# Performance work log

Hardware: AMD Instinct MI355X
Metric: run time of the kernel (lower is better)

Reference implementation:

```python
import jax, jax.numpy as jnp
import numpy as np

B, T, D, H = 64, 512, 1024, 1024


def setup_inputs() -> dict:
    key = jax.random.key(0)
    k1, k2, k3, k4, k5 = jax.random.split(key, 5)
    return {
        "c0": jax.random.normal(k1, (B, H), jnp.float32),
        "h0": jax.random.normal(k2, (B, H), jnp.float32),
        "x": jax.random.normal(k3, (B, T, D), jnp.float32),
        "Wi": jax.random.normal(k4, (D, 4 * H), jnp.float32) * 0.02,
        "Wh": jax.random.normal(k5, (H, 4 * H), jnp.float32) * 0.02,
        "b": jnp.zeros((4 * H,), jnp.float32),
    }


def reference(c0, h0, x, Wi, Wh, b):
    # flax OptimizedLSTMCell: fused gates = x @ Wi (no bias) + h @ Wh + b,
    # split into i, f, g, o; carry = (c, h).
    def step(carry, xt):
        c, h = carry
        gates = xt @ Wi + h @ Wh + b  # [B, 4H]
        i, f, g, o = jnp.split(gates, 4, axis=-1)
        new_c = jax.nn.sigmoid(f) * c + jax.nn.sigmoid(i) * jnp.tanh(g)
        new_h = jax.nn.sigmoid(o) * jnp.tanh(new_c)
        return (new_c, new_h), new_h

    # scan over time axis (original uses in_axes=1/out_axes=1)
    (cT, hT), ys = jax.lax.scan(step, (c0, h0), jnp.swapaxes(x, 0, 1))
    return cT, hT, jnp.swapaxes(ys, 0, 1)  # final carry + [B, T, H] outputs
```

## Files before the change

kernel.cpp:

```cpp
#include <hip/hip_runtime.h>

#define B_ 64
#define T_ 512
#define D_ 1024
#define H_ 1024
#define NG_ 4096

typedef __attribute__((ext_vector_type(8))) short short8v;
typedef __attribute__((ext_vector_type(4))) float f32x4;

static __device__ inline unsigned short f2bf(float f) {
  unsigned u = __float_as_uint(f);
  return (unsigned short)((u + 0x7fffu + ((u >> 16) & 1u)) >> 16);
}
static __device__ inline float bf2f(unsigned short s) {
  return __uint_as_float((unsigned)s << 16);
}

static __device__ inline float4 llc_load4(const float* p) {
  float4 r;
  asm volatile("global_load_dwordx4 %0, %1, off sc0 sc1" : "=v"(r) : "v"(p));
  return r;
}
static __device__ inline void llc_store1(float* p, float v) {
  asm volatile("global_store_dword %0, %1, off sc0 sc1" :: "v"(p), "v"(v) : "memory");
}
static __device__ inline void llc_store_u16(unsigned short* p, unsigned v) {
  asm volatile("global_store_short %0, %1, off sc0 sc1" :: "v"(p), "v"(v) : "memory");
}
#define VMWAIT(N)                                          \
  asm volatile("s_waitcnt vmcnt(" #N ")" ::: "memory");    \
  __builtin_amdgcn_sched_barrier(0);

__global__ __launch_bounds__(256) void k_trans_h_fwd(const float* __restrict__ h,
                                                     float* __restrict__ hT) {
  int idx = blockIdx.x * 256 + threadIdx.x;
  int b = idx & 63;
  int k = idx >> 6;
  hT[idx] = h[b * H_ + k];
}
__global__ __launch_bounds__(256) void k_trans_h_back(const float* __restrict__ hT,
                                                      float* __restrict__ h) {
  int idx = blockIdx.x * 256 + threadIdx.x;
  int k = idx & (H_ - 1);
  int b = idx >> 10;
  h[idx] = hT[k * 64 + b];
}

__global__ __launch_bounds__(256) void k_init_hfrag(const float* __restrict__ h0,
                                                    unsigned short* __restrict__ hf) {
  const int idx = blockIdx.x * 256 + threadIdx.x;
  const int j = idx & 7;
  const int l = (idx >> 3) & 63;
  const int bt = (idx >> 9) & 3;
  const int kt = idx >> 11;
  const int b = bt * 16 + (l & 15);
  const int k = kt * 32 + ((l >> 4) << 3) + j;
  hf[idx] = f2bf(h0[b * H_ + k]);
}

__global__ __launch_bounds__(256) void k_h_final(const float* __restrict__ ys,
                                                 float* __restrict__ h) {
  const int idx = blockIdx.x * 256 + threadIdx.x;
  const int b = idx >> 10;
  const int k = idx & 1023;
  h[idx] = ys[(size_t)b * (T_ * H_) + (size_t)(T_ - 1) * H_ + k];
}

__global__ __launch_bounds__(256) void k_prep_w(const float* __restrict__ Wi,
                                                short8v* __restrict__ wh) {
  const int idx = blockIdx.x * 256 + threadIdx.x;
  const int l = idx & 63;
  const int kt = (idx >> 6) & 31;
  const int nt = idx >> 11;
  const int n = nt * 16 + (l & 15);
  const int k = kt * 32 + ((l >> 4) << 3);
  short8v h;
#pragma unroll
  for (int j = 0; j < 8; ++j) h[j] = (short)f2bf(Wi[(size_t)(k + j) * NG_ + n]);
  wh[idx] = h;
}

__global__ __launch_bounds__(256) void k_prep_x(const float* __restrict__ x,
                                                short8v* __restrict__ xh,
                                                int t0) {
  const int idx = blockIdx.x * 256 + threadIdx.x;
  const int l = idx & 63;
  const int bt = (idx >> 6) & 3;
  const int kt = (idx >> 8) & 31;
  const int tt = idx >> 13;
  const int b = bt * 16 + (l & 15);
  const int k = kt * 32 + ((l >> 4) << 3);
  const float* p = x + ((size_t)b * T_ + (t0 + tt)) * D_ + k;
  const float4 f0 = *(const float4*)p;
  const float4 f1 = *(const float4*)(p + 4);
  const float v[8] = {f0.x, f0.y, f0.z, f0.w, f1.x, f1.y, f1.z, f1.w};
  short8v h;
#pragma unroll
  for (int j = 0; j < 8; ++j) h[j] = (short)f2bf(v[j]);
  xh[idx] = h;
}

__global__ __launch_bounds__(512, 2) void k_fused(
    const float* __restrict__ Wh,
    const short8v* __restrict__ xh,
    const short8v* __restrict__ wh,
    const float* __restrict__ bias,
    float* __restrict__ gx,
    unsigned short* __restrict__ hfA, unsigned short* __restrict__ hfB,
    float* __restrict__ c_state,
    float* __restrict__ ys,
    unsigned* __restrict__ bar,
    int t0, int tc) {
  extern __shared__ char smemc[];

  const int tid = threadIdx.x;
  const int l = tid & 63;
  const int w = tid >> 6;
  const int bid = blockIdx.x;
  unsigned* done = bar + 512;

  if (bid >= 128) {
    const int gi = bid - 128;
    const int oct = gi & 7;
    const int nt0 = oct * 32 + w * 4;
    for (int j = gi; j < tc * 8; j += 128) {
      const int tt = j >> 3;
      f32x4 acc[4][4];
#pragma unroll
      for (int i = 0; i < 4; ++i)
#pragma unroll
        for (int q = 0; q < 4; ++q) acc[i][q] = (f32x4){0.f, 0.f, 0.f, 0.f};

#pragma unroll 2
      for (int kt = 0; kt < 32; ++kt) {
        short8v ah[4], bh[4];
#pragma unroll
        for (int bt = 0; bt < 4; ++bt)
          ah[bt] = xh[((size_t)(tt * 32 + kt) * 4 + bt) * 64 + l];
#pragma unroll
        for (int q = 0; q < 4; ++q)
          bh[q] = wh[((size_t)(nt0 + q) * 32 + kt) * 64 + l];
#pragma unroll
        for (int bt = 0; bt < 4; ++bt)
#pragma unroll
          for (int q = 0; q < 4; ++q)
            acc[bt][q] = __builtin_amdgcn_mfma_f32_16x16x32_bf16(ah[bt], bh[q], acc[bt][q], 0, 0, 0);
      }

#pragma unroll
      for (int q = 0; q < 4; ++q) {
        const int n = (nt0 + q) * 16 + (l & 15);
        const int g = n >> 10;
        const int cb = (n & 1023) >> 2;
        const int c = n & 3;
        const float bv = bias[n];
#pragma unroll
        for (int bt = 0; bt < 4; ++bt)
#pragma unroll
          for (int r = 0; r < 4; ++r) {
            const int b = bt * 16 + (l >> 4) * 4 + r;
            llc_store1(gx + (((size_t)tt * 256 + cb) * 64 + b) * 16 + c * 4 + g,
                       acc[bt][q][r] + bv);
          }
      }
      asm volatile("s_waitcnt vmcnt(0)" ::: "memory");
      __syncthreads();
      if (tid == 0)
        __hip_atomic_fetch_add(&done[t0 + tt], 1u, __ATOMIC_RELAXED,
                               __HIP_MEMORY_SCOPE_AGENT);
    }
    return;
  }

  short8v* wldsh = (short8v*)smemc;
  short8v* wldsl = wldsh + 4096;
  float* red = (float*)(wldsl + 4096);

  const int bt = w & 3;
  const int kt0 = (w >> 2) * 16;
  const int hbase = bid * 8;

  for (int idx = tid; idx < 4096; idx += 512) {
    const int ct = idx >> 11;
    const int rem = idx & 2047;
    const int kt = rem >> 6;
    const int ll = rem & 63;
    const int cc = ll & 15;
    const int gc = ct * 16 + cc;
    const int c = gc >> 2, g = gc & 3;
    const int kb = kt * 32 + ((ll >> 4) << 3);
    short8v hi, lo;
#pragma unroll
    for (int j = 0; j < 8; ++j) {
      const float v = Wh[(size_t)(kb + j) * NG_ + g * H_ + hbase + c];
      const unsigned short bh = f2bf(v);
      hi[j] = (short)bh;
      lo[j] = (short)f2bf(v - bf2f(bh));
    }
    wldsh[idx] = hi;
    wldsl[idx] = lo;
  }

  const int eb = tid >> 3;
  const int c8 = tid & 7;
  const int hcol = hbase + c8;
  const size_t sOff = (((size_t)((hcol >> 5) * 4 + (eb >> 4)) * 64 +
                        ((((hcol & 31) >> 3) << 4) | (eb & 15))) * 8 + (hcol & 7));
  const int cbq = bid * 2 + (c8 >> 2);
  const int ebt = eb >> 4;
  const int erb = eb & 15;
  const int err_ = erb & 3;
  const int elrow = (erb >> 2) << 4;
  const int ect = c8 >> 2;

  float c_reg = c_state[eb * H_ + hcol];

  if (tid == 0) {
    while (__hip_atomic_load(&done[t0], __ATOMIC_RELAXED, __HIP_MEMORY_SCOPE_AGENT) < 8u)
      __builtin_amdgcn_s_sleep(1);
  }
  __syncthreads();

  for (int tt = 0; tt < tc; ++tt) {
    const int t = t0 + tt;
    const unsigned short* __restrict__ hf_in = (t & 1) ? hfB : hfA;
    unsigned short* __restrict__ hf_out = (t & 1) ? hfA : hfB;

    float4 gxv = llc_load4(gx + (((size_t)tt * 256 + cbq) * 64 + eb) * 16 + (c8 & 3) * 4);
    float4 aq[16];
#pragma unroll
    for (int q = 0; q < 16; ++q)
      aq[q] = llc_load4((const float*)(hf_in + (((size_t)(kt0 + q) * 4 + bt) * 64 + l) * 8));

    f32x4 acc0 = (f32x4){0.f, 0.f, 0.f, 0.f};
    f32x4 acc1 = (f32x4){0.f, 0.f, 0.f, 0.f};

#define STEPQ(Q, VM)                                                        \
    { const short8v bh0 = wldsh[(kt0 + (Q)) * 64 + l];                      \
      const short8v bl0 = wldsl[(kt0 + (Q)) * 64 + l];                      \
      const short8v bh1 = wldsh[2048 + (kt0 + (Q)) * 64 + l];               \
      const short8v bl1 = wldsl[2048 + (kt0 + (Q)) * 64 + l];               \
      VMWAIT(VM)                                                            \
      const short8v av = __builtin_bit_cast(short8v, aq[Q]);                \
      acc0 = __builtin_amdgcn_mfma_f32_16x16x32_bf16(av, bh0, acc0, 0, 0, 0); \
      acc0 = __builtin_amdgcn_mfma_f32_16x16x32_bf16(av, bl0, acc0, 0, 0, 0); \
      acc1 = __builtin_amdgcn_mfma_f32_16x16x32_bf16(av, bh1, acc1, 0, 0, 0); \
      acc1 = __builtin_amdgcn_mfma_f32_16x16x32_bf16(av, bl1, acc1, 0, 0, 0); }
    STEPQ(0, 15)  STEPQ(1, 14)  STEPQ(2, 13)  STEPQ(3, 12)
    STEPQ(4, 11)  STEPQ(5, 10)  STEPQ(6, 9)   STEPQ(7, 8)
    STEPQ(8, 7)   STEPQ(9, 6)   STEPQ(10, 5)  STEPQ(11, 4)
    STEPQ(12, 3)  STEPQ(13, 2)  STEPQ(14, 1)  STEPQ(15, 0)
#undef STEPQ

#pragma unroll
    for (int r = 0; r < 4; ++r) {
      red[((w * 2 + 0) * 64 + l) * 4 + r] = acc0[r];
      red[((w * 2 + 1) * 64 + l) * 4 + r] = acc1[r];
    }
    __syncthreads();

    {
      const float* gp = &gxv.x;
      float v[4];
#pragma unroll
      for (int g = 0; g < 4; ++g) {
        const int cc = (c8 & 3) * 4 + g;
        const int lp = elrow | cc;
        v[g] = gp[g] +
               red[(((0 * 4 + ebt) * 2 + ect) * 64 + lp) * 4 + err_] +
               red[(((1 * 4 + ebt) * 2 + ect) * 64 + lp) * 4 + err_];
      }
      const float si = 1.f / (1.f + expf(-v[0]));
      const float sf = 1.f / (1.f + expf(-v[1]));
      const float gt = tanhf(v[2]);
      const float so = 1.f / (1.f + expf(-v[3]));
      const float cn = sf * c_reg + si * gt;
      const float hn = so * tanhf(cn);
      c_reg = cn;
      llc_store_u16(hf_out + sOff, (unsigned)f2bf(hn));
      ys[(size_t)eb * (T_ * H_) + (size_t)t * H_ + hcol] = hn;
    }

    asm volatile("s_waitcnt vmcnt(0)" ::: "memory");
    __syncthreads();
    if (tid == 0) {
      __hip_atomic_fetch_add(&bar[(bid & 7) << 5], 1u,
                             __ATOMIC_RELAXED, __HIP_MEMORY_SCOPE_AGENT);
      const unsigned tgt = 128u * (unsigned)(t + 1);
      unsigned s;
      do {
        s = 0;
#pragma unroll
        for (int i = 0; i < 8; ++i)
          s += __hip_atomic_load(&bar[i << 5], __ATOMIC_RELAXED,
                                 __HIP_MEMORY_SCOPE_AGENT);
        if (s < tgt) __builtin_amdgcn_s_sleep(1);
      } while (s < tgt);
    }
    if (tid == 64 && tt + 1 < tc) {
      while (__hip_atomic_load(&done[t + 1], __ATOMIC_RELAXED,
                               __HIP_MEMORY_SCOPE_AGENT) < 8u)
        __builtin_amdgcn_s_sleep(1);
    }
    __syncthreads();
  }

  c_state[eb * H_ + hcol] = c_reg;
}

#define FMA16F(V, W0, W1, W2, W3)               \
  acc[0][0] = fmaf((V), (W0).x, acc[0][0]);     \
  acc[1][0] = fmaf((V), (W0).y, acc[1][0]);     \
  acc[2][0] = fmaf((V), (W0).z, acc[2][0]);     \
  acc[3][0] = fmaf((V), (W0).w, acc[3][0]);     \
  acc[0][1] = fmaf((V), (W1).x, acc[0][1]);     \
  acc[1][1] = fmaf((V), (W1).y, acc[1][1]);     \
  acc[2][1] = fmaf((V), (W1).z, acc[2][1]);     \
  acc[3][1] = fmaf((V), (W1).w, acc[3][1]);     \
  acc[0][2] = fmaf((V), (W2).x, acc[0][2]);     \
  acc[1][2] = fmaf((V), (W2).y, acc[1][2]);     \
  acc[2][2] = fmaf((V), (W2).z, acc[2][2]);     \
  acc[3][2] = fmaf((V), (W2).w, acc[3][2]);     \
  acc[0][3] = fmaf((V), (W3).x, acc[0][3]);     \
  acc[1][3] = fmaf((V), (W3).y, acc[1][3]);     \
  acc[2][3] = fmaf((V), (W3).z, acc[2][3]);     \
  acc[3][3] = fmaf((V), (W3).w, acc[3][3]);

__global__ __launch_bounds__(512, 2) void k_lstm_step_fused(
    const float* __restrict__ xsrc, const float* __restrict__ Wi,
    const float* __restrict__ Wh, const float* __restrict__ bias,
    const float* __restrict__ hT_in, float* __restrict__ hT_out,
    float* __restrict__ c_state, float* __restrict__ ys_t) {
  __shared__ float red[8 * 64 * 17];
  const int tid = threadIdx.x;
  const int lane = tid & 63;
  const int w = tid >> 6;
  const int hbase = blockIdx.x * 4;
  float acc[4][4];
#pragma unroll
  for (int c = 0; c < 4; ++c)
#pragma unroll
    for (int g = 0; g < 4; ++g) acc[c][g] = 0.f;
  const int k0 = w * 128;
#pragma unroll 2
  for (int k = k0; k < k0 + 128; ++k) {
    const float hv = hT_in[k * 64 + lane];
    const float xv = xsrc[(size_t)lane * (T_ * D_) + k];
    const float4 wh0 = *(const float4*)(Wh + (size_t)k * NG_ + 0 * H_ + hbase);
    const float4 wh1 = *(const float4*)(Wh + (size_t)k * NG_ + 1 * H_ + hbase);
    const float4 wh2 = *(const float4*)(Wh + (size_t)k * NG_ + 2 * H_ + hbase);
    const float4 wh3 = *(const float4*)(Wh + (size_t)k * NG_ + 3 * H_ + hbase);
    FMA16F(hv, wh0, wh1, wh2, wh3)
    const float4 wi0 = *(const float4*)(Wi + (size_t)k * NG_ + 0 * H_ + hbase);
    const float4 wi1 = *(const float4*)(Wi + (size_t)k * NG_ + 1 * H_ + hbase);
    const float4 wi2 = *(const float4*)(Wi + (size_t)k * NG_ + 2 * H_ + hbase);
    const float4 wi3 = *(const float4*)(Wi + (size_t)k * NG_ + 3 * H_ + hbase);
    FMA16F(xv, wi0, wi1, wi2, wi3)
  }
#pragma unroll
  for (int c = 0; c < 4; ++c)
#pragma unroll
    for (int g = 0; g < 4; ++g) red[(w * 64 + lane) * 17 + c * 4 + g] = acc[c][g];
  __syncthreads();
  if (tid < 256) {
    const int b = tid >> 2;
    const int c = tid & 3;
    const int h = hbase + c;
    float v[4];
#pragma unroll
    for (int g = 0; g < 4; ++g) {
      float s = bias[g * H_ + h];
#pragma unroll
      for (int ww = 0; ww < 8; ++ww) s += red[(ww * 64 + b) * 17 + c * 4 + g];
      v[g] = s;
    }
    const float cold = c_state[b * H_ + h];
    const float si = 1.f / (1.f + expf(-v[0]));
    const float sf = 1.f / (1.f + expf(-v[1]));
    const float gt = tanhf(v[2]);
    const float so = 1.f / (1.f + expf(-v[3]));
    const float cn = sf * cold + si * gt;
    const float hn = so * tanhf(cn);
    c_state[b * H_ + h] = cn;
    hT_out[h * 64 + b] = hn;
    ys_t[(size_t)b * (T_ * H_) + h] = hn;
  }
}

extern "C" void kernel_launch(void* const* d_in, const int* in_sizes, int n_in,
                              void* d_out, int out_size, void* d_ws, size_t ws_size,
                              hipStream_t stream) {
  const float* c0   = (const float*)d_in[0];
  const float* h0   = (const float*)d_in[1];
  const float* x    = (const float*)d_in[2];
  const float* Wi   = (const float*)d_in[3];
  const float* Wh   = (const float*)d_in[4];
  const float* bias = (const float*)d_in[5];

  float* out     = (float*)d_out;
  float* c_state = out;
  float* h_final = out + B_ * H_;
  float* ys      = out + 2 * B_ * H_;

  const size_t hbytes = (size_t)B_ * H_ * sizeof(float);
  char* ws = (char*)d_ws;
  unsigned* bar = (unsigned*)ws;
  char* hbufA = ws + 8192;
  char* hbufB = hbufA + hbytes;
  const size_t wfrag_n = (size_t)256 * 32 * 64;
  short8v* wh = (short8v*)(hbufB + hbytes);
  char* chunkbase = (char*)(wh + wfrag_n);

  const size_t xfrag_t = (size_t)32 * 4 * 64;
  const size_t per_t = xfrag_t * sizeof(short8v) + (size_t)256 * 64 * 16 * sizeof(float);
  const size_t fixed = (size_t)(chunkbase - ws);
  size_t avail = (ws_size > fixed) ? ws_size - fixed : 0;
  int Tc = (int)(avail / per_t);
  if (Tc > T_) Tc = T_;

  hipMemsetAsync(bar, 0, 8192, stream);
  hipMemcpyAsync(c_state, c0, hbytes, hipMemcpyDeviceToDevice, stream);

  if (Tc >= 1) {
    unsigned short* hfA = (unsigned short*)hbufA;
    unsigned short* hfB = (unsigned short*)hbufB;

    k_init_hfrag<<<256, 256, 0, stream>>>(h0, hfA);
    k_prep_w<<<2048, 256, 0, stream>>>(Wi, wh);

    const unsigned smem = (4096 + 4096) * 16 + 4096 * 4;

    for (int t0 = 0; t0 < T_; t0 += Tc) {
      const int tc = (T_ - t0 < Tc) ? (T_ - t0) : Tc;
      short8v* xh = (short8v*)chunkbase;
      float* gxbuf = (float*)(xh + (size_t)tc * xfrag_t);

      k_prep_x<<<tc * 32, 256, 0, stream>>>(x, xh, t0);

      int t0v = t0, tcv = tc;
      void* args[] = {(void*)&Wh,  (void*)&xh,   (void*)&wh,
                      (void*)&bias, (void*)&gxbuf,
                      (void*)&hfA, (void*)&hfB,  (void*)&c_state,
                      (void*)&ys,  (void*)&bar,  (void*)&t0v, (void*)&tcv};
      hipLaunchCooperativeKernel((void*)k_fused, dim3(256), dim3(512), args,
                                 smem, stream);
    }
    k_h_final<<<256, 256, 0, stream>>>(ys, h_final);
  } else {
    float* hA = (float*)hbufA;
    float* hB = (float*)hbufB;
    k_trans_h_fwd<<<B_ * H_ / 256, 256, 0, stream>>>(h0, hA);
    for (int t = 0; t < T_; ++t) {
      const float* hin = (t & 1) ? hB : hA;
      float* hout      = (t & 1) ? hA : hB;
      k_lstm_step_fused<<<256, 512, 0, stream>>>(
          x + (size_t)t * D_, Wi, Wh, bias, hin, hout, c_state,
          ys + (size_t)t * H_);
    }
    k_trans_h_back<<<B_ * H_ / 256, 256, 0, stream>>>(hA, h_final);
  }
}
```

Baseline: 2.808 ms.

## Drop bf16 hi/lo split of Wh and halve recurrent blocks to 64

The recurrent Wh slice is now stored in LDS as a single bf16 copy instead of a high/low bf16 pair, so each block can hold 16 hidden columns instead of 8 and the recurrent phase runs on 64 blocks instead of 128. The freed 64 blocks join the input-projection (x@Wi) workers, and the grid barrier target drops to 64 arrivals per step. This cuts the number of blocks that must meet at each timestep's barrier and removes half the recurrent MFMAs, but it loses the extra precision of the split-bf16 Wh and doubles the per-block gate epilogue work. It also adds an extra LDS reduction round with more __syncthreads.

```diff
diff --git a/kernel.cpp b/kernel.cpp
--- a/kernel.cpp
+++ b/kernel.cpp
@@ -120,11 +120,11 @@
   const int bid = blockIdx.x;
   unsigned* done = bar + 512;
 
-  if (bid >= 128) {
-    const int gi = bid - 128;
+  if (bid >= 64) {
+    const int gi = bid - 64;
     const int oct = gi & 7;
     const int nt0 = oct * 32 + w * 4;
-    for (int j = gi; j < tc * 8; j += 128) {
+    for (int j = gi; j < tc * 8; j += 192) {
       const int tt = j >> 3;
       f32x4 acc[4][4];
 #pragma unroll
@@ -173,48 +173,48 @@
     return;
   }
 
-  short8v* wldsh = (short8v*)smemc;
-  short8v* wldsl = wldsh + 4096;
-  float* red = (float*)(wldsl + 4096);
+  short8v* wlds = (short8v*)smemc;
+  float* red = (float*)(wlds + 8192);
 
   const int bt = w & 3;
   const int kt0 = (w >> 2) * 16;
-  const int hbase = bid * 8;
-
-  for (int idx = tid; idx < 4096; idx += 512) {
+  const int hbase = bid * 16;
+
+  for (int idx = tid; idx < 8192; idx += 512) {
     const int ct = idx >> 11;
     const int rem = idx & 2047;
     const int kt = rem >> 6;
     const int ll = rem & 63;
-    const int cc = ll & 15;
-    const int gc = ct * 16 + cc;
-    const int c = gc >> 2, g = gc & 3;
+    const int gc = ct * 16 + (ll & 15);
+    const int hl = gc >> 2;
+    const int g = gc & 3;
     const int kb = kt * 32 + ((ll >> 4) << 3);
-    short8v hi, lo;
-#pragma unroll
-    for (int j = 0; j < 8; ++j) {
-      const float v = Wh[(size_t)(kb + j) * NG_ + g * H_ + hbase + c];
-      const unsigned short bh = f2bf(v);
-      hi[j] = (short)bh;
-      lo[j] = (short)f2bf(v - bf2f(bh));
-    }
-    wldsh[idx] = hi;
-    wldsl[idx] = lo;
+    short8v hi;
+#pragma unroll
+    for (int j = 0; j < 8; ++j)
+      hi[j] = (short)f2bf(Wh[(size_t)(kb + j) * NG_ + g * H_ + hbase + hl]);
+    wlds[idx] = hi;
   }
 
   const int eb = tid >> 3;
   const int c8 = tid & 7;
-  const int hcol = hbase + c8;
-  const size_t sOff = (((size_t)((hcol >> 5) * 4 + (eb >> 4)) * 64 +
-                        ((((hcol & 31) >> 3) << 4) | (eb & 15))) * 8 + (hcol & 7));
-  const int cbq = bid * 2 + (c8 >> 2);
-  const int ebt = eb >> 4;
-  const int erb = eb & 15;
-  const int err_ = erb & 3;
-  const int elrow = (erb >> 2) << 4;
-  const int ect = c8 >> 2;
-
-  float c_reg = c_state[eb * H_ + hcol];
+  const int hcolA = hbase + c8;
+  const int hcolB = hbase + 8 + c8;
+  const size_t sOffA = (((size_t)((hcolA >> 5) * 4 + (eb >> 4)) * 64 +
+                         ((((hcolA & 31) >> 3) << 4) | (eb & 15))) * 8 + (hcolA & 7));
+  const size_t sOffB = (((size_t)((hcolB >> 5) * 4 + (eb >> 4)) * 64 +
+                         ((((hcolB & 31) >> 3) << 4) | (eb & 15))) * 8 + (hcolB & 7));
+  const int cbA = bid * 4 + (c8 >> 2);
+  const int cbB = bid * 4 + 2 + (c8 >> 2);
+  const int goff = (c8 & 3) * 4;
+  const int bt_e = eb >> 4;
+  const int r_e = eb & 3;
+  const int lbase = ((eb & 15) >> 2) << 4;
+  const int coff = (c8 & 3) * 4;
+  const int ctr = c8 >> 2;
+
+  float c_regA = c_state[eb * H_ + hcolA];
+  float c_regB = c_state[eb * H_ + hcolB];
 
   if (tid == 0) {
     while (__hip_atomic_load(&done[t0], __ATOMIC_RELAXED, __HIP_MEMORY_SCOPE_AGENT) < 8u)
@@ -227,7 +227,8 @@
     const unsigned short* __restrict__ hf_in = (t & 1) ? hfB : hfA;
     unsigned short* __restrict__ hf_out = (t & 1) ? hfA : hfB;
 
-    float4 gxv = llc_load4(gx + (((size_t)tt * 256 + cbq) * 64 + eb) * 16 + (c8 & 3) * 4);
+    float4 gxvA = llc_load4(gx + (((size_t)tt * 256 + cbA) * 64 + eb) * 16 + goff);
+    float4 gxvB = llc_load4(gx + (((size_t)tt * 256 + cbB) * 64 + eb) * 16 + goff);
     float4 aq[16];
 #pragma unroll
     for (int q = 0; q < 16; ++q)
@@ -235,18 +236,20 @@
 
     f32x4 acc0 = (f32x4){0.f, 0.f, 0.f, 0.f};
     f32x4 acc1 = (f32x4){0.f, 0.f, 0.f, 0.f};
+    f32x4 acc2 = (f32x4){0.f, 0.f, 0.f, 0.f};
+    f32x4 acc3 = (f32x4){0.f, 0.f, 0.f, 0.f};
 
 #define STEPQ(Q, VM)                                                        \
-    { const short8v bh0 = wldsh[(kt0 + (Q)) * 64 + l];                      \
-      const short8v bl0 = wldsl[(kt0 + (Q)) * 64 + l];                      \
-      const short8v bh1 = wldsh[2048 + (kt0 + (Q)) * 64 + l];               \
-      const short8v bl1 = wldsl[2048 + (kt0 + (Q)) * 64 + l];               \
+    { const short8v b0 = wlds[(kt0 + (Q)) * 64 + l];                        \
+      const short8v b1 = wlds[2048 + (kt0 + (Q)) * 64 + l];                 \
+      const short8v b2 = wlds[4096 + (kt0 + (Q)) * 64 + l];                 \
+      const short8v b3 = wlds[6144 + (kt0 + (Q)) * 64 + l];                 \
       VMWAIT(VM)                                                            \
       const short8v av = __builtin_bit_cast(short8v, aq[Q]);                \
-      acc0 = __builtin_amdgcn_mfma_f32_16x16x32_bf16(av, bh0, acc0, 0, 0, 0); \
-      acc0 = __builtin_amdgcn_mfma_f32_16x16x32_bf16(av, bl0, acc0, 0, 0, 0); \
-      acc1 = __builtin_amdgcn_mfma_f32_16x16x32_bf16(av, bh1, acc1, 0, 0, 0); \
-      acc1 = __builtin_amdgcn_mfma_f32_16x16x32_bf16(av, bl1, acc1, 0, 0, 0); }
+      acc0 = __builtin_amdgcn_mfma_f32_16x16x32_bf16(av, b0, acc0, 0, 0, 0); \
+      acc1 = __builtin_amdgcn_mfma_f32_16x16x32_bf16(av, b1, acc1, 0, 0, 0); \
+      acc2 = __builtin_amdgcn_mfma_f32_16x16x32_bf16(av, b2, acc2, 0, 0, 0); \
+      acc3 = __builtin_amdgcn_mfma_f32_16x16x32_bf16(av, b3, acc3, 0, 0, 0); }
     STEPQ(0, 15)  STEPQ(1, 14)  STEPQ(2, 13)  STEPQ(3, 12)
     STEPQ(4, 11)  STEPQ(5, 10)  STEPQ(6, 9)   STEPQ(7, 8)
     STEPQ(8, 7)   STEPQ(9, 6)   STEPQ(10, 5)  STEPQ(11, 4)
@@ -259,27 +262,53 @@
       red[((w * 2 + 1) * 64 + l) * 4 + r] = acc1[r];
     }
     __syncthreads();
-
     {
-      const float* gp = &gxv.x;
+      const float* gp = &gxvA.x;
       float v[4];
 #pragma unroll
       for (int g = 0; g < 4; ++g) {
-        const int cc = (c8 & 3) * 4 + g;
-        const int lp = elrow | cc;
+        const int lp = lbase | (coff + g);
         v[g] = gp[g] +
-               red[(((0 * 4 + ebt) * 2 + ect) * 64 + lp) * 4 + err_] +
-               red[(((1 * 4 + ebt) * 2 + ect) * 64 + lp) * 4 + err_];
+               red[(((0 + bt_e) * 2 + ctr) * 64 + lp) * 4 + r_e] +
+               red[(((4 + bt_e) * 2 + ctr) * 64 + lp) * 4 + r_e];
       }
       const float si = 1.f / (1.f + expf(-v[0]));
       const float sf = 1.f / (1.f + expf(-v[1]));
       const float gt = tanhf(v[2]);
       const float so = 1.f / (1.f + expf(-v[3]));
-      const float cn = sf * c_reg + si * gt;
+      const float cn = sf * c_regA + si * gt;
       const float hn = so * tanhf(cn);
-      c_reg = cn;
-      llc_store_u16(hf_out + sOff, (unsigned)f2bf(hn));
-      ys[(size_t)eb * (T_ * H_) + (size_t)t * H_ + hcol] = hn;
+      c_regA = cn;
+      llc_store_u16(hf_out + sOffA, (unsigned)f2bf(hn));
+      ys[(size_t)eb * (T_ * H_) + (size_t)t * H_ + hcolA] = hn;
+    }
+    __syncthreads();
+
+#pragma unroll
+    for (int r = 0; r < 4; ++r) {
+      red[((w * 2 + 0) * 64 + l) * 4 + r] = acc2[r];
+      red[((w * 2 + 1) * 64 + l) * 4 + r] = acc3[r];
+    }
+    __syncthreads();
+    {
+      const float* gp = &gxvB.x;
+      float v[4];
+#pragma unroll
+      for (int g = 0; g < 4; ++g) {
+        const int lp = lbase | (coff + g);
+        v[g] = gp[g] +
+               red[(((0 + bt_e) * 2 + ctr) * 64 + lp) * 4 + r_e] +
+               red[(((4 + bt_e) * 2 + ctr) * 64 + lp) * 4 + r_e];
+      }
+      const float si = 1.f / (1.f + expf(-v[0]));
+      const float sf = 1.f / (1.f + expf(-v[1]));
+      const float gt = tanhf(v[2]);
+      const float so = 1.f / (1.f + expf(-v[3]));
+      const float cn = sf * c_regB + si * gt;
+      const float hn = so * tanhf(cn);
+      c_regB = cn;
+      llc_store_u16(hf_out + sOffB, (unsigned)f2bf(hn));
+      ys[(size_t)eb * (T_ * H_) + (size_t)t * H_ + hcolB] = hn;
     }
 
     asm volatile("s_waitcnt vmcnt(0)" ::: "memory");
@@ -287,7 +316,7 @@
     if (tid == 0) {
       __hip_atomic_fetch_add(&bar[(bid & 7) << 5], 1u,
                              __ATOMIC_RELAXED, __HIP_MEMORY_SCOPE_AGENT);
-      const unsigned tgt = 128u * (unsigned)(t + 1);
+      const unsigned tgt = 64u * (unsigned)(t + 1);
       unsigned s;
       do {
         s = 0;
@@ -306,7 +335,8 @@
     __syncthreads();
   }
 
-  c_state[eb * H_ + hcol] = c_reg;
+  c_state[eb * H_ + hcolA] = c_regA;
+  c_state[eb * H_ + hcolB] = c_regB;
 }
 
 #define FMA16F(V, W0, W1, W2, W3)               \
@@ -429,7 +459,7 @@
     k_init_hfrag<<<256, 256, 0, stream>>>(h0, hfA);
     k_prep_w<<<2048, 256, 0, stream>>>(Wi, wh);
 
-    const unsigned smem = (4096 + 4096) * 16 + 4096 * 4;
+    const unsigned smem = 8192 * 16 + 4096 * 4;
 
     for (int t0 = 0; t0 < T_; t0 += Tc) {
       const int tc = (T_ - t0 < Tc) ? (T_ - t0) : Tc;
```

After: 3.204 ms. +14.1%, slower.
